# Kernel tuning notes

Measured on AMD Instinct MI355X. Metric: run time of the kernel, lower is better.

Reference implementation:

```python
import jax, jax.numpy as jnp
import numpy as np

B, L, ENC_DIM, DEC_DIM, ATTN_DIM = 64, 2048, 1024, 1024, 512


def setup_inputs() -> dict:
    key = jax.random.key(0)
    ks = jax.random.split(key, 8)
    s_enc = 1.0 / np.sqrt(ENC_DIM)
    s_dec = 1.0 / np.sqrt(DEC_DIM)
    s_full = 1.0 / np.sqrt(ATTN_DIM)
    return {
        "encoder_out": jax.random.normal(ks[0], (B, L, ENC_DIM), jnp.float32),
        "decoder_hidden": jax.random.normal(ks[1], (B, DEC_DIM), jnp.float32),
        "We_w": jax.random.uniform(ks[2], (ENC_DIM, ATTN_DIM), jnp.float32, -s_enc, s_enc),
        "We_b": jax.random.uniform(ks[3], (ATTN_DIM,), jnp.float32, -s_enc, s_enc),
        "Wd_w": jax.random.uniform(ks[4], (DEC_DIM, ATTN_DIM), jnp.float32, -s_dec, s_dec),
        "Wd_b": jax.random.uniform(ks[5], (ATTN_DIM,), jnp.float32, -s_dec, s_dec),
        "Wf_w": jax.random.uniform(ks[6], (ATTN_DIM,), jnp.float32, -s_full, s_full),
        "Wf_b": jax.random.uniform(ks[7], (), jnp.float32, -s_full, s_full),
    }


def reference(encoder_out, decoder_hidden, We_w, We_b, Wd_w, Wd_b, Wf_w, Wf_b):
    # enc_attn: [B, L, A]; dec_attn: [B, A]
    enc_attn = jnp.einsum("ble,ea->bla", encoder_out, We_w) + We_b
    dec_attn = decoder_hidden @ Wd_w + Wd_b
    # additive score -> scalar per (B, L)
    hidden = jax.nn.relu(enc_attn + dec_attn[:, None, :])
    attn = jnp.einsum("bla,a->bl", hidden, Wf_w) + Wf_b
    alpha = jax.nn.softmax(attn, axis=1)  # over sequence dim
    weighted = jnp.einsum("ble,bl->be", encoder_out, alpha)
    return (weighted, alpha)
```

## Files before the change

kernel.cpp:

```cpp
#include <hip/hip_runtime.h>
#include <stdint.h>

#define B_BATCH 64
#define L_SEQ 2048
#define E_DIM 1024
#define A_DIM 512

typedef __attribute__((ext_vector_type(4))) float f32x4;
typedef __attribute__((ext_vector_type(8))) short bf16x8;
typedef __attribute__((ext_vector_type(2))) unsigned int u32x2;
typedef __attribute__((ext_vector_type(4))) unsigned int u32x4;

__device__ __forceinline__ unsigned short f2bf(float f) {
  unsigned u = __float_as_uint(f);
  u = (u + 0x7fffu + ((u >> 16) & 1u)) >> 16;
  return (unsigned short)u;
}

__device__ __forceinline__ u32x2 packbf(f32x4 v) {
  u32x2 r;
  r.x = (unsigned)f2bf(v.x) | ((unsigned)f2bf(v.y) << 16);
  r.y = (unsigned)f2bf(v.z) | ((unsigned)f2bf(v.w) << 16);
  return r;
}

__device__ __forceinline__ int kperm(int kg) { return (kg & 3) * 2 + (kg >> 2); }

__device__ __forceinline__ void gload_lds16(const void* g, void* l) {
  __builtin_amdgcn_global_load_lds(
      (const __attribute__((address_space(1))) unsigned int*)(uintptr_t)g,
      (__attribute__((address_space(3))) unsigned int*)(unsigned)(uintptr_t)l,
      16, 0, 0);
}

#define ASTRIDE 80
#define ABYTES (128 * ASTRIDE)
#define NB_COLS 256
#define BBYTES (NB_COLS * ASTRIDE)
#define BUFBYTES (ABYTES + BBYTES)
#define BCHUNK 40960

__global__ void prep_we_kernel(const float* __restrict__ We, char* __restrict__ wsB) {
  int t = blockIdx.x * 256 + threadIdx.x;
  int n = t & 511;
  int kgl = t >> 9;
  int e0 = kgl * 4;
  int kb = e0 >> 5;
  int kg = (e0 & 31) >> 2;
  unsigned lo = (unsigned)f2bf(We[(size_t)(e0 + 0) * A_DIM + n]) |
                ((unsigned)f2bf(We[(size_t)(e0 + 1) * A_DIM + n]) << 16);
  unsigned hi = (unsigned)f2bf(We[(size_t)(e0 + 2) * A_DIM + n]) |
                ((unsigned)f2bf(We[(size_t)(e0 + 3) * A_DIM + n]) << 16);
  u32x2 val; val.x = lo; val.y = hi;
  *(u32x2*)(wsB + (size_t)kb * BCHUNK + n * ASTRIDE + kperm(kg) * 8) = val;
}

__global__ void dec_comb_kernel(const float* __restrict__ dh, const float* __restrict__ Wd,
                                const float* __restrict__ Wdb, const float* __restrict__ Web,
                                float* __restrict__ dcomb) {
  __shared__ float sh[1024];
  const int b = blockIdx.x, tid = threadIdx.x;
  for (int i = tid; i < 1024; i += 256) sh[i] = dh[b * 1024 + i];
  __syncthreads();
  const int a = blockIdx.y * 256 + tid;
  float acc = Wdb[a] + Web[a];
#pragma unroll 4
  for (int e = 0; e < 1024; ++e) acc += sh[e] * Wd[(size_t)e * A_DIM + a];
  dcomb[b * A_DIM + a] = acc;
}

__global__ __launch_bounds__(256, 2) void score_gemm_kernel(
    const float* __restrict__ enc, const char* __restrict__ wsB,
    const float* __restrict__ dcomb, const float* __restrict__ wf,
    float* __restrict__ scoreOut) {
  __shared__ __align__(16) char smem[2 * BUFBYTES];
  __shared__ float s_score[128];

  const int tid = threadIdx.x;
  const int lane = tid & 63;
  const int w = tid >> 6;
  const int g = lane >> 4;
  const int nl = lane & 15;

  const int bid = (int)blockIdx.x;
  const int lbid = (bid & 7) * 256 + (bid >> 3);
  const int split = lbid & 1;
  const int rowblk = lbid >> 1;
  const int row0 = rowblk * 128;
  const int bb = row0 >> 11;

  if (tid < 128) s_score[tid] = 0.0f;

  const float* encA = enc + (size_t)row0 * E_DIM;

  int aoff[8];
  int boff[4];
#pragma unroll
  for (int rt = 0; rt < 8; ++rt) aoff[rt] = (rt * 16 + nl) * ASTRIDE + g * 16;
#pragma unroll
  for (int ct = 0; ct < 4; ++ct) boff[ct] = ABYTES + (w * 64 + ct * 16 + nl) * ASTRIDE + g * 16;

  const int ar0 = tid >> 2, ac = tid & 3;
  const int ar1 = ar0 + 64;
  const int aw0 = ar0 * ASTRIDE + ac * 16;
  const int aw1 = ar1 * ASTRIDE + ac * 16;
  const float* asrc0 = encA + (size_t)ar0 * E_DIM + ac * 4;
  const float* asrc1 = encA + (size_t)ar1 * E_DIM + ac * 4;

  const char* bsrc = wsB + split * (NB_COLS * ASTRIDE);

  f32x4 acc[8][4];
#pragma unroll
  for (int rt = 0; rt < 8; ++rt)
#pragma unroll
    for (int ct = 0; ct < 4; ++ct) {
      f32x4 z = {0.f, 0.f, 0.f, 0.f};
      acc[rt][ct] = z;
    }

  {
#pragma unroll
    for (int c = 0; c < 5; ++c)
      gload_lds16(bsrc + c * 4096 + w * 1024 + lane * 16,
                  smem + ABYTES + c * 4096 + w * 1024);
    f32x4 va = *(const f32x4*)(asrc0);
    f32x4 vb = *(const f32x4*)(asrc0 + 16);
    f32x4 vc = *(const f32x4*)(asrc1);
    f32x4 vd = *(const f32x4*)(asrc1 + 16);
    u32x2 lo0 = packbf(va), hi0 = packbf(vb), lo1 = packbf(vc), hi1 = packbf(vd);
    u32x4 w0; w0.x = lo0.x; w0.y = lo0.y; w0.z = hi0.x; w0.w = hi0.y;
    u32x4 w1; w1.x = lo1.x; w1.y = lo1.y; w1.z = hi1.x; w1.w = hi1.y;
    *(u32x4*)(smem + aw0) = w0;
    *(u32x4*)(smem + aw1) = w1;
  }
  __syncthreads();

  f32x4 va, vb, vc, vd;
  for (int step = 0; step < 32; ++step) {
    const char* cur = smem + (step & 1) * BUFBYTES;
    char* nxt = smem + ((step + 1) & 1) * BUFBYTES;
    if (step < 31) {
      const int kb = step + 1;
#pragma unroll
      for (int c = 0; c < 5; ++c)
        gload_lds16(bsrc + (size_t)kb * BCHUNK + c * 4096 + w * 1024 + lane * 16,
                    nxt + ABYTES + c * 4096 + w * 1024);
      va = *(const f32x4*)(asrc0 + kb * 32);
      vb = *(const f32x4*)(asrc0 + kb * 32 + 16);
      vc = *(const f32x4*)(asrc1 + kb * 32);
      vd = *(const f32x4*)(asrc1 + kb * 32 + 16);
    }
    bf16x8 bfr[4], afr[8];
#pragma unroll
    for (int ct = 0; ct < 4; ++ct) bfr[ct] = *(const bf16x8*)(cur + boff[ct]);
#pragma unroll
    for (int rt = 0; rt < 8; ++rt) afr[rt] = *(const bf16x8*)(cur + aoff[rt]);
#pragma unroll
    for (int rt = 0; rt < 8; ++rt)
#pragma unroll
      for (int ct = 0; ct < 4; ++ct)
        acc[rt][ct] = __builtin_amdgcn_mfma_f32_16x16x32_bf16(afr[rt], bfr[ct],
                                                              acc[rt][ct], 0, 0, 0);
    if (step < 31) {
      u32x2 lo0 = packbf(va), hi0 = packbf(vb), lo1 = packbf(vc), hi1 = packbf(vd);
      u32x4 w0; w0.x = lo0.x; w0.y = lo0.y; w0.z = hi0.x; w0.w = hi0.y;
      u32x4 w1; w1.x = lo1.x; w1.y = lo1.y; w1.z = hi1.x; w1.w = hi1.y;
      *(u32x4*)(nxt + aw0) = w0;
      *(u32x4*)(nxt + aw1) = w1;
    }
    __syncthreads();
  }

  float db[4], wv[4];
#pragma unroll
  for (int ct = 0; ct < 4; ++ct) {
    int a = split * NB_COLS + w * 64 + ct * 16 + nl;
    db[ct] = dcomb[bb * A_DIM + a];
    wv[ct] = wf[a];
  }
#pragma unroll
  for (int rt = 0; rt < 8; ++rt) {
#pragma unroll
    for (int r = 0; r < 4; ++r) {
      float p = 0.f;
#pragma unroll
      for (int ct = 0; ct < 4; ++ct) {
        float h = acc[rt][ct][r] + db[ct];
        h = h > 0.f ? h : 0.f;
        p += h * wv[ct];
      }
      p += __shfl_xor(p, 1);
      p += __shfl_xor(p, 2);
      p += __shfl_xor(p, 4);
      p += __shfl_xor(p, 8);
      if (nl == 0) atomicAdd(&s_score[rt * 16 + g * 4 + r], p);
    }
  }
  __syncthreads();
  if (tid < 128) atomicAdd(&scoreOut[row0 + tid], s_score[tid]);
}

__global__ void softmax_kernel(float* __restrict__ attn) {
  __shared__ float red[8];
  const int b = blockIdx.x, tid = threadIdx.x;
  float* p = attn + b * L_SEQ;
  float v[8];
  float m = -1e30f;
#pragma unroll
  for (int i = 0; i < 8; ++i) {
    v[i] = p[tid + i * 256];
    m = fmaxf(m, v[i]);
  }
#pragma unroll
  for (int off = 1; off < 64; off <<= 1) m = fmaxf(m, __shfl_xor(m, off));
  const int wid = tid >> 6;
  if ((tid & 63) == 0) red[wid] = m;
  __syncthreads();
  m = fmaxf(fmaxf(red[0], red[1]), fmaxf(red[2], red[3]));
  float s = 0.f;
#pragma unroll
  for (int i = 0; i < 8; ++i) {
    v[i] = __expf(v[i] - m);
    s += v[i];
  }
#pragma unroll
  for (int off = 1; off < 64; off <<= 1) s += __shfl_xor(s, off);
  __syncthreads();
  if ((tid & 63) == 0) red[4 + wid] = s;
  __syncthreads();
  const float inv = 1.0f / (red[4] + red[5] + red[6] + red[7]);
#pragma unroll
  for (int i = 0; i < 8; ++i) p[tid + i * 256] = v[i] * inv;
}

__global__ void weighted_kernel(const float* __restrict__ enc, const float* __restrict__ alpha,
                                float* __restrict__ outW) {
  __shared__ float sa[256];
  const int bid = blockIdx.x;
  const int b = bid >> 3, ls = bid & 7;
  const int tid = threadIdx.x;
  sa[tid] = alpha[b * L_SEQ + ls * 256 + tid];
  __syncthreads();
  const f32x4* ep = (const f32x4*)(enc + ((size_t)(b * L_SEQ + ls * 256)) * E_DIM) + tid;
  f32x4 acc = {0.f, 0.f, 0.f, 0.f};
#pragma unroll 8
  for (int il = 0; il < 256; ++il) {
    f32x4 v = ep[(size_t)il * 256];
    float al = sa[il];
    acc.x += al * v.x;
    acc.y += al * v.y;
    acc.z += al * v.z;
    acc.w += al * v.w;
  }
  float* o = outW + b * E_DIM + tid * 4;
  atomicAdd(o + 0, acc.x);
  atomicAdd(o + 1, acc.y);
  atomicAdd(o + 2, acc.z);
  atomicAdd(o + 3, acc.w);
}

extern "C" void kernel_launch(void* const* d_in, const int* in_sizes, int n_in,
                              void* d_out, int out_size, void* d_ws, size_t ws_size,
                              hipStream_t stream) {
  const float* enc = (const float*)d_in[0];
  const float* dh = (const float*)d_in[1];
  const float* WeW = (const float*)d_in[2];
  const float* WeB = (const float*)d_in[3];
  const float* WdW = (const float*)d_in[4];
  const float* WdB = (const float*)d_in[5];
  const float* WfW = (const float*)d_in[6];

  float* out = (float*)d_out;
  float* outW = out;
  float* attn = out + B_BATCH * E_DIM;

  char* wsB = (char*)d_ws;
  float* dcomb = (float*)((char*)d_ws + 32 * (size_t)BCHUNK);

  if (ws_size < 32 * (size_t)BCHUNK + (size_t)B_BATCH * A_DIM * sizeof(float)) return;

  hipMemsetAsync(out, 0, (size_t)(B_BATCH * E_DIM + B_BATCH * L_SEQ) * sizeof(float), stream);
  prep_we_kernel<<<512, 256, 0, stream>>>(WeW, wsB);
  dec_comb_kernel<<<dim3(B_BATCH, 2), 256, 0, stream>>>(dh, WdW, WdB, WeB, dcomb);
  score_gemm_kernel<<<(B_BATCH * L_SEQ) / 128 * 2, 256, 0, stream>>>(enc, wsB, dcomb, WfW, attn);
  softmax_kernel<<<B_BATCH, 256, 0, stream>>>(attn);
  weighted_kernel<<<B_BATCH * 8, 256, 0, stream>>>(enc, attn, outW);
}
```

Baseline: 434.2 us.

## Triple-buffer score GEMM with XOR-swizzled LDS and split weighted sum finer

The score GEMM moves from a padded double-buffered LDS layout to a triple-buffered ring with an XOR-swizzled 64-byte row layout, and the prep kernel writes We to match. Global A loads are issued two steps ahead using explicit vmcnt waits and a raw s_barrier, and s_setprio is raised around the MFMA block, to hide load latency and avoid LDS bank conflicts. Separately, the weighted-sum kernel uses 64-row chunks across 4x more blocks to raise parallelism, at the cost of more atomics. The hand-written waitcnt counts are fragile and must match the number of outstanding loads exactly.

After: 408.5 us. -5.9%, faster.

```diff
diff --git a/kernel.cpp b/kernel.cpp
--- a/kernel.cpp
+++ b/kernel.cpp
@@ -24,8 +24,6 @@
   return r;
 }
 
-__device__ __forceinline__ int kperm(int kg) { return (kg & 3) * 2 + (kg >> 2); }
-
 __device__ __forceinline__ void gload_lds16(const void* g, void* l) {
   __builtin_amdgcn_global_load_lds(
       (const __attribute__((address_space(1))) unsigned int*)(uintptr_t)g,
@@ -33,12 +31,9 @@
       16, 0, 0);
 }
 
-#define ASTRIDE 80
-#define ABYTES (128 * ASTRIDE)
-#define NB_COLS 256
-#define BBYTES (NB_COLS * ASTRIDE)
-#define BUFBYTES (ABYTES + BBYTES)
-#define BCHUNK 40960
+#define BCHUNK 32768
+#define BUFB 24576
+#define ABASE 16384
 
 __global__ void prep_we_kernel(const float* __restrict__ We, char* __restrict__ wsB) {
   int t = blockIdx.x * 256 + threadIdx.x;
@@ -46,13 +41,14 @@
   int kgl = t >> 9;
   int e0 = kgl * 4;
   int kb = e0 >> 5;
-  int kg = (e0 & 31) >> 2;
+  int kg = (e0 >> 2) & 7;
   unsigned lo = (unsigned)f2bf(We[(size_t)(e0 + 0) * A_DIM + n]) |
                 ((unsigned)f2bf(We[(size_t)(e0 + 1) * A_DIM + n]) << 16);
   unsigned hi = (unsigned)f2bf(We[(size_t)(e0 + 2) * A_DIM + n]) |
                 ((unsigned)f2bf(We[(size_t)(e0 + 3) * A_DIM + n]) << 16);
   u32x2 val; val.x = lo; val.y = hi;
-  *(u32x2*)(wsB + (size_t)kb * BCHUNK + n * ASTRIDE + kperm(kg) * 8) = val;
+  int slot = (kg & 3) ^ ((n >> 1) & 3);
+  *(u32x2*)(wsB + (size_t)kb * BCHUNK + n * 64 + slot * 16 + (kg >> 2) * 8) = val;
 }
 
 __global__ void dec_comb_kernel(const float* __restrict__ dh, const float* __restrict__ Wd,
@@ -73,7 +69,7 @@
     const float* __restrict__ enc, const char* __restrict__ wsB,
     const float* __restrict__ dcomb, const float* __restrict__ wf,
     float* __restrict__ scoreOut) {
-  __shared__ __align__(16) char smem[2 * BUFBYTES];
+  __shared__ __align__(16) char smem[3 * BUFB];
   __shared__ float s_score[128];
 
   const int tid = threadIdx.x;
@@ -81,33 +77,30 @@
   const int w = tid >> 6;
   const int g = lane >> 4;
   const int nl = lane & 15;
+  const int gs = g ^ ((nl >> 1) & 3);
 
   const int bid = (int)blockIdx.x;
   const int lbid = (bid & 7) * 256 + (bid >> 3);
   const int split = lbid & 1;
-  const int rowblk = lbid >> 1;
-  const int row0 = rowblk * 128;
+  const int row0 = (lbid >> 1) * 128;
   const int bb = row0 >> 11;
 
   if (tid < 128) s_score[tid] = 0.0f;
 
   const float* encA = enc + (size_t)row0 * E_DIM;
-
-  int aoff[8];
-  int boff[4];
-#pragma unroll
-  for (int rt = 0; rt < 8; ++rt) aoff[rt] = (rt * 16 + nl) * ASTRIDE + g * 16;
-#pragma unroll
-  for (int ct = 0; ct < 4; ++ct) boff[ct] = ABYTES + (w * 64 + ct * 16 + nl) * ASTRIDE + g * 16;
+  const char* bsrc = wsB + split * 16384;
+
+  int aoff[8], boff[4];
+#pragma unroll
+  for (int rt = 0; rt < 8; ++rt) aoff[rt] = ABASE + (rt * 16 + nl) * 64 + gs * 16;
+#pragma unroll
+  for (int ct = 0; ct < 4; ++ct) boff[ct] = (w * 64 + ct * 16 + nl) * 64 + gs * 16;
 
   const int ar0 = tid >> 2, ac = tid & 3;
-  const int ar1 = ar0 + 64;
-  const int aw0 = ar0 * ASTRIDE + ac * 16;
-  const int aw1 = ar1 * ASTRIDE + ac * 16;
-  const float* asrc0 = encA + (size_t)ar0 * E_DIM + ac * 4;
-  const float* asrc1 = encA + (size_t)ar1 * E_DIM + ac * 4;
-
-  const char* bsrc = wsB + split * (NB_COLS * ASTRIDE);
+  const int aw0 = ABASE + ar0 * 64 + ((ac ^ ((ar0 >> 1) & 3)) * 16);
+  const int aw1 = aw0 + 4096;
+  const float* as0 = encA + (size_t)ar0 * E_DIM + ac * 4;
+  const float* as1 = as0 + 64 * E_DIM;
 
   f32x4 acc[8][4];
 #pragma unroll
@@ -117,64 +110,87 @@
       f32x4 z = {0.f, 0.f, 0.f, 0.f};
       acc[rt][ct] = z;
     }
-
-  {
-#pragma unroll
-    for (int c = 0; c < 5; ++c)
-      gload_lds16(bsrc + c * 4096 + w * 1024 + lane * 16,
-                  smem + ABYTES + c * 4096 + w * 1024);
-    f32x4 va = *(const f32x4*)(asrc0);
-    f32x4 vb = *(const f32x4*)(asrc0 + 16);
-    f32x4 vc = *(const f32x4*)(asrc1);
-    f32x4 vd = *(const f32x4*)(asrc1 + 16);
-    u32x2 lo0 = packbf(va), hi0 = packbf(vb), lo1 = packbf(vc), hi1 = packbf(vd);
-    u32x4 w0; w0.x = lo0.x; w0.y = lo0.y; w0.z = hi0.x; w0.w = hi0.y;
-    u32x4 w1; w1.x = lo1.x; w1.y = lo1.y; w1.z = hi1.x; w1.w = hi1.y;
-    *(u32x4*)(smem + aw0) = w0;
-    *(u32x4*)(smem + aw1) = w1;
-  }
-  __syncthreads();
-
-  f32x4 va, vb, vc, vd;
-  for (int step = 0; step < 32; ++step) {
-    const char* cur = smem + (step & 1) * BUFBYTES;
-    char* nxt = smem + ((step + 1) & 1) * BUFBYTES;
-    if (step < 31) {
-      const int kb = step + 1;
-#pragma unroll
-      for (int c = 0; c < 5; ++c)
-        gload_lds16(bsrc + (size_t)kb * BCHUNK + c * 4096 + w * 1024 + lane * 16,
-                    nxt + ABYTES + c * 4096 + w * 1024);
-      va = *(const f32x4*)(asrc0 + kb * 32);
-      vb = *(const f32x4*)(asrc0 + kb * 32 + 16);
-      vc = *(const f32x4*)(asrc1 + kb * 32);
-      vd = *(const f32x4*)(asrc1 + kb * 32 + 16);
-    }
-    bf16x8 bfr[4], afr[8];
-#pragma unroll
-    for (int ct = 0; ct < 4; ++ct) bfr[ct] = *(const bf16x8*)(cur + boff[ct]);
-#pragma unroll
-    for (int rt = 0; rt < 8; ++rt) afr[rt] = *(const bf16x8*)(cur + aoff[rt]);
-#pragma unroll
-    for (int rt = 0; rt < 8; ++rt)
-#pragma unroll
-      for (int ct = 0; ct < 4; ++ct)
-        acc[rt][ct] = __builtin_amdgcn_mfma_f32_16x16x32_bf16(afr[rt], bfr[ct],
-                                                              acc[rt][ct], 0, 0, 0);
-    if (step < 31) {
-      u32x2 lo0 = packbf(va), hi0 = packbf(vb), lo1 = packbf(vc), hi1 = packbf(vd);
-      u32x4 w0; w0.x = lo0.x; w0.y = lo0.y; w0.z = hi0.x; w0.w = hi0.y;
-      u32x4 w1; w1.x = lo1.x; w1.y = lo1.y; w1.z = hi1.x; w1.w = hi1.y;
-      *(u32x4*)(nxt + aw0) = w0;
-      *(u32x4*)(nxt + aw1) = w1;
-    }
-    __syncthreads();
-  }
+  f32x4 ra[2][4];
+
+#define STAGE_B(kb_, dst_)                                                  \
+  do {                                                                      \
+    _Pragma("unroll") for (int c = 0; c < 4; ++c)                           \
+        gload_lds16(bsrc + (size_t)(kb_)*BCHUNK + w * 4096 + c * 1024 +     \
+                        lane * 16,                                          \
+                    smem + (dst_) + w * 4096 + c * 1024);                   \
+  } while (0)
+
+#define LOAD_A(kb_, s_)                                 \
+  do {                                                  \
+    ra[s_][0] = *(const f32x4*)(as0 + (kb_)*32);        \
+    ra[s_][1] = *(const f32x4*)(as0 + (kb_)*32 + 16);   \
+    ra[s_][2] = *(const f32x4*)(as1 + (kb_)*32);        \
+    ra[s_][3] = *(const f32x4*)(as1 + (kb_)*32 + 16);   \
+  } while (0)
+
+#define WRITE_A(s_, dst_)                                          \
+  do {                                                             \
+    u32x2 l0 = packbf(ra[s_][0]), h0 = packbf(ra[s_][1]);          \
+    u32x2 l1 = packbf(ra[s_][2]), h1 = packbf(ra[s_][3]);          \
+    u32x4 w0; w0.x = l0.x; w0.y = l0.y; w0.z = h0.x; w0.w = h0.y;  \
+    u32x4 w1; w1.x = l1.x; w1.y = l1.y; w1.z = h1.x; w1.w = h1.y;  \
+    *(u32x4*)(smem + (dst_) + aw0) = w0;                           \
+    *(u32x4*)(smem + (dst_) + aw1) = w1;                           \
+  } while (0)
+
+#define COMPUTE(cur_)                                                        \
+  do {                                                                       \
+    bf16x8 bfr[4], afr[8];                                                   \
+    _Pragma("unroll") for (int ct = 0; ct < 4; ++ct) bfr[ct] =               \
+        *(const bf16x8*)(smem + (cur_) + boff[ct]);                          \
+    _Pragma("unroll") for (int rt = 0; rt < 8; ++rt) afr[rt] =               \
+        *(const bf16x8*)(smem + (cur_) + aoff[rt]);                          \
+    __builtin_amdgcn_s_setprio(1);                                           \
+    _Pragma("unroll") for (int rt = 0; rt < 8; ++rt)                         \
+        _Pragma("unroll") for (int ct = 0; ct < 4; ++ct) acc[rt][ct] =       \
+            __builtin_amdgcn_mfma_f32_16x16x32_bf16(afr[rt], bfr[ct],        \
+                                                    acc[rt][ct], 0, 0, 0);   \
+    __builtin_amdgcn_s_setprio(0);                                           \
+  } while (0)
+
+  LOAD_A(0, 0);
+  STAGE_B(0, 0);
+  LOAD_A(1, 1);
+  asm volatile("s_waitcnt vmcnt(8)" ::: "memory");
+  WRITE_A(0, 0);
+
+  int b0 = 0, b1 = BUFB, b2 = 2 * BUFB;
+#pragma unroll 6
+  for (int t = 0; t < 30; ++t) {
+    STAGE_B(t + 1, b1);
+    LOAD_A(t + 2, t & 1);
+    asm volatile("s_waitcnt vmcnt(8)" ::: "memory");
+    WRITE_A((t + 1) & 1, b1);
+    asm volatile("s_waitcnt lgkmcnt(0)" ::: "memory");
+    asm volatile("s_barrier" ::: "memory");
+    COMPUTE(b0);
+    int tmp = b0; b0 = b1; b1 = b2; b2 = tmp;
+  }
+  STAGE_B(31, b1);
+  asm volatile("s_waitcnt vmcnt(4)" ::: "memory");
+  WRITE_A(1, b1);
+  asm volatile("s_waitcnt lgkmcnt(0)" ::: "memory");
+  asm volatile("s_barrier" ::: "memory");
+  COMPUTE(b0);
+  { int tmp = b0; b0 = b1; b1 = b2; b2 = tmp; }
+  asm volatile("s_waitcnt vmcnt(0) lgkmcnt(0)" ::: "memory");
+  asm volatile("s_barrier" ::: "memory");
+  COMPUTE(b0);
+
+#undef STAGE_B
+#undef LOAD_A
+#undef WRITE_A
+#undef COMPUTE
 
   float db[4], wv[4];
 #pragma unroll
   for (int ct = 0; ct < 4; ++ct) {
-    int a = split * NB_COLS + w * 64 + ct * 16 + nl;
+    int a = split * 256 + w * 64 + ct * 16 + nl;
     db[ct] = dcomb[bb * A_DIM + a];
     wv[ct] = wf[a];
   }
@@ -235,16 +251,16 @@
 
 __global__ void weighted_kernel(const float* __restrict__ enc, const float* __restrict__ alpha,
                                 float* __restrict__ outW) {
-  __shared__ float sa[256];
+  __shared__ float sa[64];
   const int bid = blockIdx.x;
-  const int b = bid >> 3, ls = bid & 7;
+  const int b = bid >> 5, ls = bid & 31;
   const int tid = threadIdx.x;
-  sa[tid] = alpha[b * L_SEQ + ls * 256 + tid];
-  __syncthreads();
-  const f32x4* ep = (const f32x4*)(enc + ((size_t)(b * L_SEQ + ls * 256)) * E_DIM) + tid;
+  if (tid < 64) sa[tid] = alpha[b * L_SEQ + ls * 64 + tid];
+  __syncthreads();
+  const f32x4* ep = (const f32x4*)(enc + ((size_t)(b * L_SEQ + ls * 64)) * E_DIM) + tid;
   f32x4 acc = {0.f, 0.f, 0.f, 0.f};
 #pragma unroll 8
-  for (int il = 0; il < 256; ++il) {
+  for (int il = 0; il < 64; ++il) {
     f32x4 v = ep[(size_t)il * 256];
     float al = sa[il];
     acc.x += al * v.x;
@@ -284,5 +300,5 @@
   dec_comb_kernel<<<dim3(B_BATCH, 2), 256, 0, stream>>>(dh, WdW, WdB, WeB, dcomb);
   score_gemm_kernel<<<(B_BATCH * L_SEQ) / 128 * 2, 256, 0, stream>>>(enc, wsB, dcomb, WfW, attn);
   softmax_kernel<<<B_BATCH, 256, 0, stream>>>(attn);
-  weighted_kernel<<<B_BATCH * 8, 256, 0, stream>>>(enc, attn, outW);
-}
+  weighted_kernel<<<B_BATCH * 32, 256, 0, stream>>>(enc, attn, outW);
+}
```
